# Kernel optimization log

Hardware: AMD Instinct MI355X
Metric: run time of the kernel (lower is better)

## Reference

```python
import jax, jax.numpy as jnp
import numpy as np


def setup_inputs() -> dict:
    key = jax.random.key(0)
    k1, k2, k3, k4 = jax.random.split(key, 4)
    B, OPT, IN, OUT = 16384, 64, 128, 128
    stddev = 1.0 / np.sqrt(IN)
    inputs = jax.random.normal(k1, (B, IN), dtype=jnp.float32)
    # haiku TruncatedNormal(stddev) init approximated with truncated normal
    w = jax.random.truncated_normal(k2, -2.0, 2.0, (OPT, IN, OUT), dtype=jnp.float32) * stddev
    b = jnp.zeros((OPT, OUT), dtype=jnp.float32)  # init=zeros; use random for a nontrivial check
    b = jax.random.normal(k3, (OPT, OUT), dtype=jnp.float32) * 0.02
    indices = jax.random.randint(k4, (B,), 0, OPT, dtype=jnp.int64)
    return {"inputs": inputs, "w": w, "b": b, "indices": indices}


def reference(inputs, w, b, indices):
    # out[i] = inputs[i] @ w[indices[i]] + b[indices[i]]
    # Faithful to vmap(jnp.dot)(inputs, w[indices]): gather per-example weight
    # matrices then batched matvec.
    wg = w[indices]                              # [B, IN, OUT] gathered weights
    out = jnp.einsum('bi,bio->bo', inputs, wg)   # [B, OUT]
    return out + b[indices]
```

## Files before the change

### kernel.cpp

```cpp
#include <hip/hip_runtime.h>


#define B_TOT     16384
#define NOPT      64
#define DIN       128
#define DOUT      128
#define NSLICE    8
#define SLICE_LEN (B_TOT / NSLICE)
#define NTHREADS  256
#define SPN       132

typedef __attribute__((ext_vector_type(8))) short  short8;
typedef __attribute__((ext_vector_type(4))) float  floatx4;

static __device__ __forceinline__ short f2bf(float f) {
    union { float f; unsigned u; } v; v.f = f;
    unsigned r = v.u + 0x7fffu + ((v.u >> 16) & 1u);
    return (short)(r >> 16);
}

__global__ __launch_bounds__(NTHREADS, 4)
void multilinear_kernel(const float* __restrict__ x,
                        const float* __restrict__ w,
                        const float* __restrict__ bias,
                        const int*   __restrict__ idx,
                        float* __restrict__ out) {
    __shared__ __align__(16) unsigned short s_w[DIN * SPN];
    __shared__ unsigned short s_list[SLICE_LEN];
    __shared__ int s_cnt;

    const int o = blockIdx.x & (NOPT - 1);
    const int s = blockIdx.x >> 6;
    const int t = threadIdx.x;

    if (t == 0) s_cnt = 0;
    __syncthreads();

    const float* wo = w + (size_t)o * (DIN * DOUT);
    #pragma unroll
    for (int it = 0; it < 16; ++it) {
        const int e = it * NTHREADS + t;
        const int k = e >> 5;
        const int c = e & 31;
        float4 v = ((const float4*)wo)[e];
        ushort4 h;
        h.x = (unsigned short)f2bf(v.x); h.y = (unsigned short)f2bf(v.y);
        h.z = (unsigned short)f2bf(v.z); h.w = (unsigned short)f2bf(v.w);
        *(ushort4*)(&s_w[k * SPN + c * 4]) = h;
    }

    const int base = s * SLICE_LEN;
    const int4* ip = (const int4*)(idx + base);
    #pragma unroll
    for (int it = 0; it < SLICE_LEN / (4 * NTHREADS); ++it) {
        const int e = it * NTHREADS + t;
        int4 v = ip[e];
        const int i0 = base + e * 4;
        if (v.x == o) s_list[atomicAdd(&s_cnt, 1)] = (unsigned short)(i0 + 0);
        if (v.y == o) s_list[atomicAdd(&s_cnt, 1)] = (unsigned short)(i0 + 1);
        if (v.z == o) s_list[atomicAdd(&s_cnt, 1)] = (unsigned short)(i0 + 2);
        if (v.w == o) s_list[atomicAdd(&s_cnt, 1)] = (unsigned short)(i0 + 3);
    }
    __syncthreads();

    const int count = s_cnt;
    if (count == 0) return;

    const int wave = t >> 6;
    const int lane = t & 63;
    const int l15  = lane & 15;
    const int quad = lane >> 4;

    const int n0 = (wave * 2) * 16 + l15;
    const int n1 = n0 + 16;

    short8 bf[4][2];
    #pragma unroll
    for (int kb = 0; kb < 4; ++kb) {
        #pragma unroll
        for (int j = 0; j < 8; ++j) {
            const int k = kb * 32 + quad * 8 + j;
            bf[kb][0][j] = (short)s_w[k * SPN + n0];
            bf[kb][1][j] = (short)s_w[k * SPN + n1];
        }
    }

    const float bv0 = bias[o * DOUT + n0];
    const float bv1 = bias[o * DOUT + n1];

    const int mtiles = (count + 15) >> 4;
    for (int mt = 0; mt < mtiles; ++mt) {
        const int am = mt * 16 + l15;
        const int arid = s_list[am < count ? am : count - 1];
        const float* xr = x + (size_t)arid * DIN;

        floatx4 acc0 = {0.f, 0.f, 0.f, 0.f};
        floatx4 acc1 = {0.f, 0.f, 0.f, 0.f};
        #pragma unroll
        for (int kb = 0; kb < 4; ++kb) {
            const int k0 = kb * 32 + quad * 8;
            float4 xa = *(const float4*)(xr + k0);
            float4 xb = *(const float4*)(xr + k0 + 4);
            short8 af;
            af[0] = f2bf(xa.x); af[1] = f2bf(xa.y);
            af[2] = f2bf(xa.z); af[3] = f2bf(xa.w);
            af[4] = f2bf(xb.x); af[5] = f2bf(xb.y);
            af[6] = f2bf(xb.z); af[7] = f2bf(xb.w);
            acc0 = __builtin_amdgcn_mfma_f32_16x16x32_bf16(af, bf[kb][0], acc0, 0, 0, 0);
            acc1 = __builtin_amdgcn_mfma_f32_16x16x32_bf16(af, bf[kb][1], acc1, 0, 0, 0);
        }

        #pragma unroll
        for (int r = 0; r < 4; ++r) {
            const int m = mt * 16 + quad * 4 + r;
            if (m < count) {
                const int rid = s_list[m];
                out[(size_t)rid * DOUT + n0] = acc0[r] + bv0;
                out[(size_t)rid * DOUT + n1] = acc1[r] + bv1;
            }
        }
    }
}

extern "C" void kernel_launch(void* const* d_in, const int* in_sizes, int n_in,
                              void* d_out, int out_size, void* d_ws, size_t ws_size,
                              hipStream_t stream) {
    const float* x    = (const float*)d_in[0];
    const float* w    = (const float*)d_in[1];
    const float* bias = (const float*)d_in[2];
    const int*   idx  = (const int*)d_in[3];
    float* out        = (float*)d_out;

    multilinear_kernel<<<NOPT * NSLICE, NTHREADS, 0, stream>>>(x, w, bias, idx, out);
}
```

Baseline: 74.73 us.

## Split output columns across two blocks per option-slice to double grid parallelism

Each block now computes only 64 of the 128 output columns for its option and batch slice, so the launch grid doubles. Each wave handles one 16-column tile instead of two, and the per-block weight staging and shared-memory footprint are halved. The cost is that the index scan and the gathered input-row reads are duplicated across the two column halves.

```diff
diff --git a/kernel.cpp b/kernel.cpp
--- a/kernel.cpp
+++ b/kernel.cpp
@@ -8,7 +8,7 @@
 #define NSLICE    8
 #define SLICE_LEN (B_TOT / NSLICE)
 #define NTHREADS  256
-#define SPN       132
+#define SPN       68
 
 typedef __attribute__((ext_vector_type(8))) short  short8;
 typedef __attribute__((ext_vector_type(4))) float  floatx4;
@@ -29,24 +29,26 @@
     __shared__ unsigned short s_list[SLICE_LEN];
     __shared__ int s_cnt;
 
-    const int o = blockIdx.x & (NOPT - 1);
-    const int s = blockIdx.x >> 6;
+    const int bid = blockIdx.x;
+    const int o = bid & (NOPT - 1);
+    const int s = (bid >> 6) & (NSLICE-1);
+    const int h = bid >> 9;
     const int t = threadIdx.x;
 
     if (t == 0) s_cnt = 0;
     __syncthreads();
 
-    const float* wo = w + (size_t)o * (DIN * DOUT);
+    const float* wo = w + (size_t)o * (DIN * DOUT) + h * 64;
     #pragma unroll
-    for (int it = 0; it < 16; ++it) {
+    for (int it = 0; it < 8; ++it) {
         const int e = it * NTHREADS + t;
-        const int k = e >> 5;
-        const int c = e & 31;
-        float4 v = ((const float4*)wo)[e];
-        ushort4 h;
-        h.x = (unsigned short)f2bf(v.x); h.y = (unsigned short)f2bf(v.y);
-        h.z = (unsigned short)f2bf(v.z); h.w = (unsigned short)f2bf(v.w);
-        *(ushort4*)(&s_w[k * SPN + c * 4]) = h;
+        const int k = e >> 4;
+        const int c = e & 15;
+        float4 v = *(const float4*)(wo + (size_t)k * DOUT + c * 4);
+        ushort4 hh;
+        hh.x = (unsigned short)f2bf(v.x); hh.y = (unsigned short)f2bf(v.y);
+        hh.z = (unsigned short)f2bf(v.z); hh.w = (unsigned short)f2bf(v.w);
+        *(ushort4*)(&s_w[k * SPN + c * 4]) = hh;
     }
 
     const int base = s * SLICE_LEN;
@@ -71,22 +73,17 @@
     const int l15  = lane & 15;
     const int quad = lane >> 4;
 
-    const int n0 = (wave * 2) * 16 + l15;
-    const int n1 = n0 + 16;
+    const int nloc  = wave * 16 + l15;
+    const int nglob = h * 64 + nloc;
 
-    short8 bf[4][2];
+    short8 bf[4];
     #pragma unroll
-    for (int kb = 0; kb < 4; ++kb) {
+    for (int kb = 0; kb < 4; ++kb)
         #pragma unroll
-        for (int j = 0; j < 8; ++j) {
-            const int k = kb * 32 + quad * 8 + j;
-            bf[kb][0][j] = (short)s_w[k * SPN + n0];
-            bf[kb][1][j] = (short)s_w[k * SPN + n1];
-        }
-    }
+        for (int j = 0; j < 8; ++j)
+            bf[kb][j] = (short)s_w[(kb * 32 + quad * 8 + j) * SPN + nloc];
 
-    const float bv0 = bias[o * DOUT + n0];
-    const float bv1 = bias[o * DOUT + n1];
+    const float bv = bias[o * DOUT + nglob];
 
     const int mtiles = (count + 15) >> 4;
     for (int mt = 0; mt < mtiles; ++mt) {
@@ -94,8 +91,7 @@
         const int arid = s_list[am < count ? am : count - 1];
         const float* xr = x + (size_t)arid * DIN;
 
-        floatx4 acc0 = {0.f, 0.f, 0.f, 0.f};
-        floatx4 acc1 = {0.f, 0.f, 0.f, 0.f};
+        floatx4 acc = {0.f, 0.f, 0.f, 0.f};
         #pragma unroll
         for (int kb = 0; kb < 4; ++kb) {
             const int k0 = kb * 32 + quad * 8;
@@ -106,8 +102,7 @@
             af[2] = f2bf(xa.z); af[3] = f2bf(xa.w);
             af[4] = f2bf(xb.x); af[5] = f2bf(xb.y);
             af[6] = f2bf(xb.z); af[7] = f2bf(xb.w);
-            acc0 = __builtin_amdgcn_mfma_f32_16x16x32_bf16(af, bf[kb][0], acc0, 0, 0, 0);
-            acc1 = __builtin_amdgcn_mfma_f32_16x16x32_bf16(af, bf[kb][1], acc1, 0, 0, 0);
+            acc = __builtin_amdgcn_mfma_f32_16x16x32_bf16(af, bf[kb], acc, 0, 0, 0);
         }
 
         #pragma unroll
@@ -115,8 +110,7 @@
             const int m = mt * 16 + quad * 4 + r;
             if (m < count) {
                 const int rid = s_list[m];
-                out[(size_t)rid * DOUT + n0] = acc0[r] + bv0;
-                out[(size_t)rid * DOUT + n1] = acc1[r] + bv1;
+                out[(size_t)rid * DOUT + nglob] = acc[r] + bv;
             }
         }
     }
@@ -131,5 +125,5 @@
     const int*   idx  = (const int*)d_in[3];
     float* out        = (float*)d_out;
 
-    multilinear_kernel<<<NOPT * NSLICE, NTHREADS, 0, stream>>>(x, w, bias, idx, out);
+    multilinear_kernel<<<NOPT * NSLICE * 2, NTHREADS, 0, stream>>>(x, w, bias, idx, out);
 }
```

After: 79.36 us. +6.2%, slower.
